# Optimization experiments

Measured on AMD Instinct MI355X. Metric: run time of the kernel, lower is better.

The kernel has to match this reference:

```python
import jax, jax.numpy as jnp
import numpy as np
from jax import lax


def _maxpool_same(x, k):
    # stride-1 max pool with symmetric padding p=(k-1)//2, pad value -inf
    # (matches torch max_pool2d implicit -inf padding)
    p = (k - 1) // 2
    return lax.reduce_window(
        x,
        -jnp.inf,
        lax.max,
        window_dimensions=(1, 1, k, k),
        window_strides=(1, 1, 1, 1),
        padding=[(0, 0), (0, 0), (p, p), (p, p)],
    )


def setup_inputs() -> dict:
    key = jax.random.key(0)
    x = jax.random.normal(key, (16, 256, 64, 64), dtype=jnp.float32)
    return {"x": x}


def reference(x):
    # SPP: concat(x, maxpool5(x), maxpool9(x), maxpool13(x)) along channels
    x1 = _maxpool_same(x, 5)
    x2 = _maxpool_same(x, 9)
    x3 = _maxpool_same(x, 13)
    return jnp.concatenate([x, x1, x2, x3], axis=1)  # [B, 4C, H, W]
```

## Files before the change

kernel.cpp:

```cpp
#include <hip/hip_runtime.h>
#include <math.h>

#define TPB 256
#define W 64
#define H 64
#define LDSW 68

typedef float f32x4 __attribute__((ext_vector_type(4)));

__device__ __forceinline__ void p1_rest(const f32x4 v[4], float* __restrict__ s,
                                        float* __restrict__ outimg, int tid) {
    const int  lane = tid & 63;
    const int  lm1 = (lane - 1) & 63;
    const int  lp1 = (lane + 1) & 63;
    const bool qlo = (lane & 15) == 0;
    const bool qhi = (lane & 15) == 15;
    const float NEG = -INFINITY;
    f32x4* o4 = (f32x4*)outimg;
    #pragma unroll
    for (int i = 0; i < 4; ++i) {
        const int idx = tid + TPB * i;
        f32x4 t = v[i];
        __builtin_nontemporal_store(t, o4 + idx);
        float e0 = __shfl(t.z, lm1, 64);
        float e1 = __shfl(t.w, lm1, 64);
        float e6 = __shfl(t.x, lp1, 64);
        float e7 = __shfl(t.y, lp1, 64);
        if (qlo) { e0 = NEG; e1 = NEG; }
        if (qhi) { e6 = NEG; e7 = NEG; }
        const float e2 = t.x, e3 = t.y, e4 = t.z, e5 = t.w;
        const float p0 = fmaxf(e0, e1), p1 = fmaxf(e1, e2), p2 = fmaxf(e2, e3);
        const float p3 = fmaxf(e3, e4), p4 = fmaxf(e4, e5), p5 = fmaxf(e5, e6);
        f32x4 r;
        r.x = fmaxf(fmaxf(p0, p2), e4);
        r.y = fmaxf(fmaxf(p1, p3), e5);
        r.z = fmaxf(fmaxf(p2, p4), e6);
        r.w = fmaxf(fmaxf(p3, p5), e7);
        const int y = idx >> 4;
        const int q = idx & 15;
        *(f32x4*)&s[y * LDSW + 4 * q] = r;
    }
}

__device__ __forceinline__ void p2(const float* __restrict__ s,
                                   float* __restrict__ outimg, int tid) {
    const float NEG = -INFINITY;
    const size_t pstr = (size_t)256 * H * W;
    const int x  = tid & 63;
    const int y0 = (tid >> 6) << 4;
    float cv[28];
    #pragma unroll
    for (int j = 0; j < 28; ++j) {
        const int y = y0 - 6 + j;
        cv[j] = (y >= 0 && y < H) ? s[y * LDSW + x] : NEG;
    }
    float p2a[27], p4a[25], p8a[21];
    #pragma unroll
    for (int j = 0; j < 27; ++j) p2a[j] = fmaxf(cv[j], cv[j + 1]);
    #pragma unroll
    for (int j = 0; j < 25; ++j) p4a[j] = fmaxf(p2a[j], p2a[j + 2]);
    #pragma unroll
    for (int j = 0; j < 21; ++j) p8a[j] = fmaxf(p4a[j], p4a[j + 4]);

    const int xm2 = (x >= 2)  ? x - 2 : 0;
    const int xp2 = (x <= 61) ? x + 2 : 63;
    const int xm4 = (x >= 4)  ? x - 4 : 0;
    const int xp4 = (x <= 59) ? x + 4 : 63;

    float* o5  = outimg +     pstr + x;
    float* o9  = outimg + 2 * pstr + x;
    float* o13 = outimg + 3 * pstr + x;
    #pragma unroll
    for (int i = 0; i < 16; ++i) {
        const float c5  = fmaxf(p4a[i + 4], cv[i + 8]);
        const float c9  = fmaxf(p8a[i + 2], cv[i + 10]);
        const float c13 = fmaxf(p8a[i], fmaxf(p4a[i + 8], cv[i + 12]));

        __builtin_nontemporal_store(c5, o5 + (y0 + i) * W);

        const float a9 = __shfl(c9, xm2, 64);
        const float b9 = __shfl(c9, xp2, 64);
        __builtin_nontemporal_store(fmaxf(a9, b9), o9 + (y0 + i) * W);

        const float a13 = __shfl(c13, xm4, 64);
        const float b13 = __shfl(c13, xp4, 64);
        __builtin_nontemporal_store(fmaxf(fmaxf(a13, c13), b13), o13 + (y0 + i) * W);
    }
}

__global__ void spp_kernel(const float* __restrict__ in, float* __restrict__ out) {
    __shared__ __align__(16) float s_a[H * LDSW];
    __shared__ __align__(16) float s_b[H * LDSW];

    const int tid  = threadIdx.x;
    const int imgA = blockIdx.x * 2;
    const int imgB = imgA + 1;
    const size_t obaseA = (((size_t)(imgA >> 8)) * 1024 + (imgA & 255)) * (H * W);
    const size_t obaseB = (((size_t)(imgB >> 8)) * 1024 + (imgB & 255)) * (H * W);

    f32x4 va[4];
    {
        const f32x4* in4 = (const f32x4*)(in + (size_t)imgA * (H * W));
        #pragma unroll
        for (int i = 0; i < 4; ++i) va[i] = __builtin_nontemporal_load(in4 + tid + TPB * i);
    }
    p1_rest(va, s_a, out + obaseA, tid);
    __syncthreads();

    f32x4 vb[4];
    {
        const f32x4* in4 = (const f32x4*)(in + (size_t)imgB * (H * W));
        #pragma unroll
        for (int i = 0; i < 4; ++i) vb[i] = __builtin_nontemporal_load(in4 + tid + TPB * i);
    }
    p2(s_a, out + obaseA, tid);
    p1_rest(vb, s_b, out + obaseB, tid);
    __syncthreads();

    p2(s_b, out + obaseB, tid);
}

extern "C" void kernel_launch(void* const* d_in, const int* in_sizes, int n_in,
                              void* d_out, int out_size, void* d_ws, size_t ws_size,
                              hipStream_t stream) {
    const float* x = (const float*)d_in[0];
    float* out = (float*)d_out;
    spp_kernel<<<dim3(2048), dim3(TPB), 0, stream>>>(x, out);
}
```

Before: 309.7 us.

## Vectorize column pass to float4 per thread with 4x4 tiles

The vertical/horizontal pooling pass now works on 4-wide columns by 4 rows per thread instead of one column by 16 rows. It reads float4 rows from LDS and writes 128-bit nontemporal stores, fetching horizontal neighbours with lane shuffles. This cuts the per-element LDS reads and store instructions, but more shuffles are needed per output and the vertical halo overhead rises (16 rows loaded for 4 outputs). A launch_bounds hint of 2 is also added.

Result: no change. 308.9 us (-0.3%).

```diff
diff --git a/kernel.cpp b/kernel.cpp
--- a/kernel.cpp
+++ b/kernel.cpp
@@ -7,6 +7,13 @@
 #define LDSW 68
 
 typedef float f32x4 __attribute__((ext_vector_type(4)));
+
+__device__ __forceinline__ f32x4 max4(f32x4 a, f32x4 b) {
+    f32x4 r;
+    r.x = fmaxf(a.x, b.x); r.y = fmaxf(a.y, b.y);
+    r.z = fmaxf(a.z, b.z); r.w = fmaxf(a.w, b.w);
+    return r;
+}
 
 __device__ __forceinline__ void p1_rest(const f32x4 v[4], float* __restrict__ s,
                                         float* __restrict__ outimg, int tid) {
@@ -46,49 +53,67 @@
                                    float* __restrict__ outimg, int tid) {
     const float NEG = -INFINITY;
     const size_t pstr = (size_t)256 * H * W;
-    const int x  = tid & 63;
-    const int y0 = (tid >> 6) << 4;
-    float cv[28];
+    const int g    = tid & 15;
+    const int x0   = g << 2;
+    const int y0   = (tid >> 4) << 2;
+    const int lane = tid & 63;
+    const int lm1  = (lane - 1) & 63;
+    const int lp1  = (lane + 1) & 63;
+    const bool qlo = (g == 0);
+    const bool qhi = (g == 15);
+
+    f32x4 cv[16];
     #pragma unroll
-    for (int j = 0; j < 28; ++j) {
-        const int y = y0 - 6 + j;
-        cv[j] = (y >= 0 && y < H) ? s[y * LDSW + x] : NEG;
+    for (int j = 0; j < 16; ++j) {
+        const int y  = y0 - 6 + j;
+        const int yc = y < 0 ? 0 : (y > 63 ? 63 : y);
+        f32x4 v = *(const f32x4*)&s[yc * LDSW + x0];
+        if (y < 0 || y > 63) v = (f32x4){NEG, NEG, NEG, NEG};
+        cv[j] = v;
     }
-    float p2a[27], p4a[25], p8a[21];
+    f32x4 m2[15], m4[13], m8[9];
     #pragma unroll
-    for (int j = 0; j < 27; ++j) p2a[j] = fmaxf(cv[j], cv[j + 1]);
+    for (int j = 0; j < 15; ++j) m2[j] = max4(cv[j], cv[j + 1]);
     #pragma unroll
-    for (int j = 0; j < 25; ++j) p4a[j] = fmaxf(p2a[j], p2a[j + 2]);
+    for (int j = 0; j < 13; ++j) m4[j] = max4(m2[j], m2[j + 2]);
     #pragma unroll
-    for (int j = 0; j < 21; ++j) p8a[j] = fmaxf(p4a[j], p4a[j + 4]);
+    for (int j = 0; j < 9;  ++j) m8[j] = max4(m4[j], m4[j + 4]);
 
-    const int xm2 = (x >= 2)  ? x - 2 : 0;
-    const int xp2 = (x <= 61) ? x + 2 : 63;
-    const int xm4 = (x >= 4)  ? x - 4 : 0;
-    const int xp4 = (x <= 59) ? x + 4 : 63;
+    float* o5  = outimg +     pstr;
+    float* o9  = outimg + 2 * pstr;
+    float* o13 = outimg + 3 * pstr;
+    #pragma unroll
+    for (int i = 0; i < 4; ++i) {
+        const f32x4 c5  = max4(m4[i + 4], cv[i + 8]);
+        const f32x4 c9  = max4(m8[i + 2], cv[i + 10]);
+        const f32x4 c13 = max4(max4(m8[i], m4[i + 8]), cv[i + 12]);
 
-    float* o5  = outimg +     pstr + x;
-    float* o9  = outimg + 2 * pstr + x;
-    float* o13 = outimg + 3 * pstr + x;
-    #pragma unroll
-    for (int i = 0; i < 16; ++i) {
-        const float c5  = fmaxf(p4a[i + 4], cv[i + 8]);
-        const float c9  = fmaxf(p8a[i + 2], cv[i + 10]);
-        const float c13 = fmaxf(p8a[i], fmaxf(p4a[i + 8], cv[i + 12]));
+        __builtin_nontemporal_store(c5, (f32x4*)(o5 + (y0 + i) * W + x0));
 
-        __builtin_nontemporal_store(c5, o5 + (y0 + i) * W);
+        const float Lz = __shfl(c9.z, lm1, 64);
+        const float Lw = __shfl(c9.w, lm1, 64);
+        const float Rx = __shfl(c9.x, lp1, 64);
+        const float Ry = __shfl(c9.y, lp1, 64);
+        const f32x4 lh9 = qlo ? (f32x4){c9.x, c9.x, c9.x, c9.y}
+                              : (f32x4){Lz, Lw, c9.x, c9.y};
+        const f32x4 rh9 = qhi ? (f32x4){c9.z, c9.w, c9.w, c9.w}
+                              : (f32x4){c9.z, c9.w, Rx, Ry};
+        __builtin_nontemporal_store(max4(lh9, rh9), (f32x4*)(o9 + (y0 + i) * W + x0));
 
-        const float a9 = __shfl(c9, xm2, 64);
-        const float b9 = __shfl(c9, xp2, 64);
-        __builtin_nontemporal_store(fmaxf(a9, b9), o9 + (y0 + i) * W);
-
-        const float a13 = __shfl(c13, xm4, 64);
-        const float b13 = __shfl(c13, xp4, 64);
-        __builtin_nontemporal_store(fmaxf(fmaxf(a13, c13), b13), o13 + (y0 + i) * W);
+        f32x4 L13, R13;
+        L13.x = __shfl(c13.x, lm1, 64); L13.y = __shfl(c13.y, lm1, 64);
+        L13.z = __shfl(c13.z, lm1, 64); L13.w = __shfl(c13.w, lm1, 64);
+        R13.x = __shfl(c13.x, lp1, 64); R13.y = __shfl(c13.y, lp1, 64);
+        R13.z = __shfl(c13.z, lp1, 64); R13.w = __shfl(c13.w, lp1, 64);
+        const f32x4 lh13 = qlo ? (f32x4){c13.x, c13.x, c13.x, c13.x} : L13;
+        const f32x4 rh13 = qhi ? (f32x4){c13.w, c13.w, c13.w, c13.w} : R13;
+        __builtin_nontemporal_store(max4(max4(lh13, c13), rh13),
+                                    (f32x4*)(o13 + (y0 + i) * W + x0));
     }
 }
 
-__global__ void spp_kernel(const float* __restrict__ in, float* __restrict__ out) {
+__global__ __launch_bounds__(TPB, 2) void spp_kernel(const float* __restrict__ in,
+                                                     float* __restrict__ out) {
     __shared__ __align__(16) float s_a[H * LDSW];
     __shared__ __align__(16) float s_b[H * LDSW];
 
```
